# Optimization experiments

Hardware: AMD Instinct MI355X
Metric: run time of the kernel (lower is better)

Reference implementation:

```python
import jax, jax.numpy as jnp
import numpy as np

EPS = 1e-5  # torch LayerNorm default


def _ln(x, g, b):
    m = jnp.mean(x, axis=-1, keepdims=True)
    v = jnp.mean((x - m) ** 2, axis=-1, keepdims=True)
    return (x - m) / jnp.sqrt(v + EPS) * g + b


def setup_inputs() -> dict:
    key = jax.random.key(0)
    ks = jax.random.split(key, 16)
    B, C, H, S, FF, BINS = 2048, 20, 256, 64, 512, 128
    f32 = jnp.float32
    def w(k, shape, s=0.02):
        return jax.random.normal(k, shape, f32) * s
    return {
        "bitplanes": jax.random.normal(ks[0], (B, C, 8, 8), f32),
        "conv1_w": w(ks[1], (H, C, 3, 3), 0.05), "conv1_b": jnp.zeros((H,), f32),
        "conv2_w": w(ks[2], (H, H, 3, 3), 0.05), "conv2_b": jnp.zeros((H,), f32),
        "in_proj_w": w(ks[3], (3 * H, H)), "in_proj_b": jnp.zeros((3 * H,), f32),
        "out_proj_w": w(ks[4], (H, H)), "out_proj_b": jnp.zeros((H,), f32),
        "ln1_g": jnp.ones((H,), f32), "ln1_b": jnp.zeros((H,), f32),
        "ff1_w": w(ks[5], (FF, H)), "ff1_b": jnp.zeros((FF,), f32),
        "ff2_w": w(ks[6], (H, FF)), "ff2_b": jnp.zeros((H,), f32),
        "ln2_g": jnp.ones((H,), f32), "ln2_b": jnp.zeros((H,), f32),
        "be1_w": w(ks[7], (H, H * S)), "be1_b": jnp.zeros((H,), f32),
        "be2_w": w(ks[8], (H, H)), "be2_b": jnp.zeros((H,), f32),
        "L1_w": w(ks[9], (H, 3 * H)), "L1_b": jnp.zeros((H,), f32),
        "L2_w": w(ks[10], (H, H)), "L2_b": jnp.zeros((H,), f32),
        "Lln_g": jnp.ones((H,), f32), "Lln_b": jnp.zeros((H,), f32),
        "H1_w": w(ks[11], (H, 2 * H)), "H1_b": jnp.zeros((H,), f32),
        "H2_w": w(ks[12], (H, H)), "H2_b": jnp.zeros((H,), f32),
        "Hln_g": jnp.ones((H,), f32), "Hln_b": jnp.zeros((H,), f32),
        "v1_w": w(ks[13], (H, H)), "v1_b": jnp.zeros((H,), f32),
        "v2_w": w(ks[14], (BINS, H)), "v2_b": jnp.zeros((BINS,), f32),
    }


def reference(bitplanes, conv1_w, conv1_b, conv2_w, conv2_b,
              in_proj_w, in_proj_b, out_proj_w, out_proj_b,
              ln1_g, ln1_b, ff1_w, ff1_b, ff2_w, ff2_b, ln2_g, ln2_b,
              be1_w, be1_b, be2_w, be2_b,
              L1_w, L1_b, L2_w, L2_b, Lln_g, Lln_b,
              H1_w, H1_b, H2_w, H2_b, Hln_g, Hln_b,
              v1_w, v1_b, v2_w, v2_b):
    N, T, Hd, nh = 8, 8, 256, 4
    B = bitplanes.shape[0]
    dn = ('NCHW', 'OIHW', 'NCHW')
    # conv encoder on 8x8 board
    x = jax.nn.relu(jax.lax.conv_general_dilated(bitplanes, conv1_w, (1, 1), 'SAME', dimension_numbers=dn) + conv1_b[None, :, None, None])
    x = jax.nn.relu(jax.lax.conv_general_dilated(x, conv2_w, (1, 1), 'SAME', dimension_numbers=dn) + conv2_b[None, :, None, None])
    x = x.reshape(B, Hd, 64).transpose(0, 2, 1)  # [B, 64, 256]
    # TransformerEncoderLayer (post-norm, eval mode => dropout off)
    qkv = x @ in_proj_w.T + in_proj_b  # [B, 64, 768]
    q, k, v = jnp.split(qkv, 3, axis=-1)
    dh = Hd // nh
    heads = lambda t: t.reshape(B, 64, nh, dh).transpose(0, 2, 1, 3)
    q, k, v = heads(q), heads(k), heads(v)
    scale = 1.0 / float(dh) ** 0.5
    a = jax.nn.softmax(jnp.einsum('bhqd,bhkd->bhqk', q, k) * scale, axis=-1)
    o = jnp.einsum('bhqk,bhkd->bhqd', a, v).transpose(0, 2, 1, 3).reshape(B, 64, Hd)
    o = o @ out_proj_w.T + out_proj_b
    x = _ln(x + o, ln1_g, ln1_b)
    ff = jax.nn.relu(x @ ff1_w.T + ff1_b) @ ff2_w.T + ff2_b
    x = _ln(x + ff, ln2_g, ln2_b)
    xf = x.reshape(B, 64 * Hd)  # [B, 16384]
    be = jax.nn.relu(jax.nn.relu(xf @ be1_w.T + be1_b) @ be2_w.T + be2_b)

    def Lnet(zL, zH):
        h = jax.nn.relu(jnp.concatenate([zL, zH, be], axis=-1) @ L1_w.T + L1_b)
        return _ln(jax.nn.relu(h @ L2_w.T + L2_b), Lln_g, Lln_b)

    def Hnet(zH, zL):
        h = jax.nn.relu(jnp.concatenate([zH, zL], axis=-1) @ H1_w.T + H1_b)
        return _ln(jax.nn.relu(h @ H2_w.T + H2_b), Hln_g, Hln_b)

    z0 = jnp.zeros((B, Hd), x.dtype)

    def step(carry, i):
        zH, zL = carry
        zL = Lnet(zL, zH)
        zH = jnp.where((i + 1) % T == 0, Hnet(zH, zL), zH)  # H update every T steps
        return (zH, zL), None

    (zH, zL), _ = jax.lax.scan(step, (z0, z0), jnp.arange(N * T - 1))
    zL = Lnet(zL, zH)
    zH = Hnet(zH, zL)
    return jax.nn.relu(zH @ v1_w.T + v1_b) @ v2_w.T + v2_b  # [B, 128]
```

## Files before the change

kernel.cpp:

```cpp
#include <hip/hip_runtime.h>
#include <hip/hip_bf16.h>
#include <math.h>

#define DEV __device__ __forceinline__

typedef __attribute__((ext_vector_type(8))) short s16x8;
typedef __attribute__((ext_vector_type(4))) float f32x4;

DEV f32x4 MF(s16x8 a, s16x8 b, f32x4 c) {
    return __builtin_amdgcn_mfma_f32_16x16x32_bf16(a, b, c, 0, 0, 0);
}

DEV void split3(float x, unsigned short& h, unsigned short& m, unsigned short& l) {
    const unsigned u = __float_as_uint(x);
    h = (unsigned short)(u >> 16);
    const float r1 = x - __uint_as_float(u & 0xffff0000u);
    const unsigned u1 = __float_as_uint(r1);
    m = (unsigned short)(u1 >> 16);
    const float r2 = r1 - __uint_as_float(u1 & 0xffff0000u);
    l = (unsigned short)(__float_as_uint(r2) >> 16);
}

DEV void split8store(const float v[8], unsigned short* d) {
    s16x8 vh, vm, vl;
#pragma unroll
    for (int j = 0; j < 8; ++j) {
        unsigned short h, m, l;
        split3(v[j], h, m, l);
        vh[j] = (short)h; vm[j] = (short)m; vl[j] = (short)l;
    }
    *(s16x8*)(d) = vh;
    *(s16x8*)(d + 512) = vm;
    *(s16x8*)(d + 1024) = vl;
}

DEV void mfma6(f32x4& acc, s16x8 ah, s16x8 am, s16x8 al, const unsigned short* bp) {
    const s16x8 bh = *(const s16x8*)(bp);
    const s16x8 bm = *(const s16x8*)(bp + 512);
    const s16x8 bl = *(const s16x8*)(bp + 1024);
    acc = MF(ah, bh, acc);
    acc = MF(ah, bm, acc);
    acc = MF(am, bh, acc);
    acc = MF(ah, bl, acc);
    acc = MF(al, bh, acc);
    acc = MF(am, bm, acc);
}

__global__ void k_tpose(const float* __restrict__ in, float* __restrict__ out, int N, int K) {
    int total = N * K;
    for (int idx = blockIdx.x * blockDim.x + threadIdx.x; idx < total; idx += gridDim.x * blockDim.x) {
        int n = idx / K, k = idx - n * K;
        out[k * N + n] = in[idx];
    }
}

__global__ void k_wpack3(const float* __restrict__ W, unsigned short* __restrict__ WP,
                         int K, int NT, int ldw, int stride, int off) {
    const int idx = blockIdx.x * 256 + threadIdx.x;
    const int total = (K >> 5) * NT * 64;
    if (idx >= total) return;
    const int lane = idx & 63;
    const int nt = (idx >> 6) % NT;
    const int ks = idx / (64 * NT);
    const int col = nt * 16 + (lane & 15);
    const int k0 = ks * 32 + ((lane >> 4) << 3);
    const float* src = W + (size_t)col * ldw + (size_t)k0 * stride + off;
    float v[8];
#pragma unroll
    for (int j = 0; j < 8; ++j) v[j] = src[j * stride];
    split8store(v, WP + (size_t)((ks * NT + nt) * 3) * 512 + lane * 8);
}

__global__ __launch_bounds__(256) void k_conv1(const float* __restrict__ in, const float* __restrict__ w,
                                               const float* __restrict__ bias, float* __restrict__ out) {
    __shared__ __align__(16) float img[20 * 100];
    __shared__ __align__(16) float stg[16 * 260];
    const int b = blockIdx.x;
    const int t = threadIdx.x;
    for (int idx = t; idx < 2000; idx += 256) {
        int c = idx / 100, pp = idx - c * 100;
        int y = pp / 10, x = pp - y * 10;
        float v = 0.f;
        if (y >= 1 && y <= 8 && x >= 1 && x <= 8)
            v = in[((size_t)b * 20 + c) * 64 + (y - 1) * 8 + (x - 1)];
        img[idx] = v;
    }
    __syncthreads();
    const int oc = t;
    float acc[64];
    const float bz = bias[oc];
#pragma unroll
    for (int p = 0; p < 64; ++p) acc[p] = bz;
    const float* wrow = w + oc * 180;
    for (int c = 0; c < 20; ++c) {
#pragma unroll
        for (int k = 0; k < 9; ++k) {
            const int ky = k / 3, kx = k - ky * 3;
            const float wv = wrow[c * 9 + k];
            const int base = c * 100 + ky * 10 + kx;
#pragma unroll
            for (int p = 0; p < 64; ++p)
                acc[p] = fmaf(wv, img[base + p + ((p >> 3) << 1)], acc[p]);
        }
    }
#pragma unroll
    for (int cc = 0; cc < 4; ++cc) {
        __syncthreads();
#pragma unroll
        for (int p = 0; p < 16; ++p) stg[p * 260 + t] = acc[cc * 16 + p];
        __syncthreads();
        for (int idx = t; idx < 4096; idx += 256) {
            const int r = idx >> 8, c = idx & 255;
            out[((size_t)b * 64 + cc * 16 + r) * 256 + c] = fmaxf(stg[r * 260 + c], 0.f);
        }
    }
}

__global__ __launch_bounds__(256) void k_conv2mf(const float* __restrict__ a1,
                                                 const unsigned short* __restrict__ WPC2,
                                                 const float* __restrict__ bias,
                                                 float* __restrict__ xout,
                                                 unsigned short* __restrict__ xh,
                                                 unsigned short* __restrict__ xm,
                                                 unsigned short* __restrict__ xl) {
    __shared__ __align__(16) unsigned short AhS[100 * 132];
    __shared__ __align__(16) unsigned short AmS[100 * 132];
    __shared__ __align__(16) unsigned short AlS[100 * 132];
    const int b = blockIdx.x, t = threadIdx.x;
    const int wv = t >> 6, lane = t & 63;
    f32x4 acc[16];
#pragma unroll
    for (int nt = 0; nt < 16; ++nt) acc[nt] = (f32x4){0.f, 0.f, 0.f, 0.f};
    const int pl = lane & 15;
    const int py = pl >> 3, px = pl & 7;
    const int akoff = (lane >> 4) << 3;
    for (int h = 0; h < 2; ++h) {
        __syncthreads();
        for (int idx = t; idx < 12800; idx += 256) {
            const int pr = idx >> 7, c = idx & 127;
            const int Y = pr / 10, X = pr - Y * 10;
            float v = 0.f;
            if (Y >= 1 && Y <= 8 && X >= 1 && X <= 8)
                v = a1[((size_t)b * 64 + (Y - 1) * 8 + X - 1) * 256 + h * 128 + c];
            unsigned short hh, mm, ll;
            split3(v, hh, mm, ll);
            AhS[pr * 132 + c] = hh;
            AmS[pr * 132 + c] = mm;
            AlS[pr * 132 + c] = ll;
        }
        __syncthreads();
#pragma unroll
        for (int tap = 0; tap < 9; ++tap) {
            const int dy = tap / 3, dx = tap - dy * 3;
            const int prow = (wv * 2 + py + dy) * 10 + px + dx;
            const unsigned short* arh = AhS + prow * 132 + akoff;
            const unsigned short* arm = AmS + prow * 132 + akoff;
            const unsigned short* arl = AlS + prow * 132 + akoff;
#pragma unroll
            for (int ks = 0; ks < 4; ++ks) {
                const s16x8 ah = *(const s16x8*)(arh + ks * 32);
                const s16x8 am = *(const s16x8*)(arm + ks * 32);
                const s16x8 al = *(const s16x8*)(arl + ks * 32);
                const unsigned short* bp = WPC2 + (size_t)(tap * 128 + (h * 4 + ks) * 16) * 1536 + lane * 8;
#pragma unroll
                for (int nt = 0; nt < 16; ++nt) {
                    mfma6(acc[nt], ah, am, al, bp + nt * 1536);
                }
            }
        }
    }
    const int prow0 = wv * 16 + ((lane >> 4) << 2);
    const int ccol = lane & 15;
#pragma unroll
    for (int nt = 0; nt < 16; ++nt) {
        const float bz = bias[nt * 16 + ccol];
#pragma unroll
        for (int i = 0; i < 4; ++i) {
            const float v = fmaxf(acc[nt][i] + bz, 0.f);
            const size_t o = ((size_t)b * 64 + prow0 + i) * 256 + nt * 16 + ccol;
            xout[o] = v;
            unsigned short hh, mm, ll;
            split3(v, hh, mm, ll);
            xh[o] = hh;
            xm[o] = mm;
            xl[o] = ll;
        }
    }
}

__global__ __launch_bounds__(512) void k_attn2(const float* __restrict__ qkv,
                                               unsigned short* __restrict__ oh, unsigned short* __restrict__ om,
                                               unsigned short* __restrict__ ol) {
    __shared__ __align__(16) float qs[64 * 65];
    __shared__ __align__(16) float ks[64 * 68];
    __shared__ __align__(16) float vs[64 * 68];
    __shared__ float pmax[8 * 64];
    __shared__ float psum[8 * 64];
    const int b = blockIdx.x, h = blockIdx.y;
    const int t = threadIdx.x;
    for (int idx = t; idx < 1024; idx += 512) {
        const int rr = idx >> 4, cc = (idx & 15) * 4;
        const float* src = qkv + ((size_t)b * 64 + rr) * 768 + h * 64 + cc;
        const float4 q4 = *(const float4*)(src);
        const float4 k4 = *(const float4*)(src + 256);
        const float4 v4 = *(const float4*)(src + 512);
        qs[rr * 65 + cc + 0] = q4.x; qs[rr * 65 + cc + 1] = q4.y;
        qs[rr * 65 + cc + 2] = q4.z; qs[rr * 65 + cc + 3] = q4.w;
        *(float4*)(ks + rr * 68 + cc) = k4;
        *(float4*)(vs + rr * 68 + cc) = v4;
    }
    __syncthreads();
    const int r = t & 63;
    const int cg = t >> 6;
    float sc[8];
#pragma unroll
    for (int j = 0; j < 8; ++j) sc[j] = 0.f;
    for (int kk = 0; kk < 64; kk += 4) {
        float qv[4];
#pragma unroll
        for (int i = 0; i < 4; ++i) qv[i] = qs[r * 65 + kk + i];
#pragma unroll
        for (int j = 0; j < 8; ++j) {
            const float4 kv = *(const float4*)(ks + (cg * 8 + j) * 68 + kk);
            sc[j] = fmaf(qv[0], kv.x, sc[j]); sc[j] = fmaf(qv[1], kv.y, sc[j]);
            sc[j] = fmaf(qv[2], kv.z, sc[j]); sc[j] = fmaf(qv[3], kv.w, sc[j]);
        }
    }
    float pm = -1e30f;
#pragma unroll
    for (int j = 0; j < 8; ++j) { sc[j] *= 0.125f; pm = fmaxf(pm, sc[j]); }
    pmax[cg * 64 + r] = pm;
    __syncthreads();
    float m = pmax[r];
#pragma unroll
    for (int i = 1; i < 8; ++i) m = fmaxf(m, pmax[i * 64 + r]);
    float pe[8], ps = 0.f;
#pragma unroll
    for (int j = 0; j < 8; ++j) { pe[j] = __expf(sc[j] - m); ps += pe[j]; }
    psum[cg * 64 + r] = ps;
    __syncthreads();
    float den = psum[r];
#pragma unroll
    for (int i = 1; i < 8; ++i) den += psum[i * 64 + r];
    const float rden = 1.f / den;
#pragma unroll
    for (int j = 0; j < 8; ++j) qs[r * 65 + cg * 8 + j] = pe[j] * rden;
    __syncthreads();
    float oa[8];
#pragma unroll
    for (int j = 0; j < 8; ++j) oa[j] = 0.f;
    for (int c = 0; c < 64; ++c) {
        const float pv = qs[r * 65 + c];
        const float4 v0 = *(const float4*)(vs + c * 68 + cg * 8);
        const float4 v1 = *(const float4*)(vs + c * 68 + cg * 8 + 4);
        oa[0] = fmaf(pv, v0.x, oa[0]); oa[1] = fmaf(pv, v0.y, oa[1]);
        oa[2] = fmaf(pv, v0.z, oa[2]); oa[3] = fmaf(pv, v0.w, oa[3]);
        oa[4] = fmaf(pv, v1.x, oa[4]); oa[5] = fmaf(pv, v1.y, oa[5]);
        oa[6] = fmaf(pv, v1.z, oa[6]); oa[7] = fmaf(pv, v1.w, oa[7]);
    }
#pragma unroll
    for (int j = 0; j < 8; ++j) ks[r * 68 + cg * 8 + j] = oa[j];
    __syncthreads();
    for (int idx = t; idx < 4096; idx += 512) {
        const int rr = idx >> 6, dd = idx & 63;
        const float v = ks[rr * 68 + dd];
        unsigned short hh, mm, ll;
        split3(v, hh, mm, ll);
        const size_t o = ((size_t)b * 64 + rr) * 256 + h * 64 + dd;
        oh[o] = hh;
        om[o] = mm;
        ol[o] = ll;
    }
}

__global__ __launch_bounds__(256) void k_gemm_mf(
    const unsigned short* __restrict__ Ah, const unsigned short* __restrict__ Am,
    const unsigned short* __restrict__ Al,
    const unsigned short* __restrict__ WP, const float* __restrict__ bias,
    float* __restrict__ Cf, unsigned short* __restrict__ Ch, unsigned short* __restrict__ Cm,
    unsigned short* __restrict__ Cl,
    int M, int N, int K, int kChunk, int relu) {
    const int t = threadIdx.x;
    const int wv = t >> 6, lane = t & 63;
    const int row0 = blockIdx.x * 64 + wv * 16;
    const int col0 = blockIdx.y * 64;
    const int NT = N >> 4;
    const int k0 = blockIdx.z * kChunk;
    const int nks = kChunk >> 5;
    f32x4 acc[4];
#pragma unroll
    for (int nt = 0; nt < 4; ++nt) acc[nt] = (f32x4){0.f, 0.f, 0.f, 0.f};
    const int arow = row0 + (lane & 15);
    const size_t aoff = (size_t)arow * K + k0 + ((lane >> 4) << 3);
    const unsigned short* aph = Ah + aoff;
    const unsigned short* apm = Am + aoff;
    const unsigned short* apl = Al + aoff;
    const unsigned short* bp = WP + ((size_t)((k0 >> 5) * NT + (col0 >> 4))) * 1536 + lane * 8;
    const size_t bstride = (size_t)NT * 1536;
    for (int ks = 0; ks < nks; ++ks) {
        const s16x8 ah = *(const s16x8*)aph;
        const s16x8 am = *(const s16x8*)apm;
        const s16x8 al = *(const s16x8*)apl;
        aph += 32; apm += 32; apl += 32;
#pragma unroll
        for (int nt = 0; nt < 4; ++nt) {
            mfma6(acc[nt], ah, am, al, bp + nt * 1536);
        }
        bp += bstride;
    }
    const int crow = row0 + ((lane >> 4) << 2);
    const int ccol = col0 + (lane & 15);
    float bz[4];
#pragma unroll
    for (int nt = 0; nt < 4; ++nt) bz[nt] = bias ? bias[ccol + nt * 16] : 0.f;
    if (Ch) {
#pragma unroll
        for (int nt = 0; nt < 4; ++nt) {
#pragma unroll
            for (int i = 0; i < 4; ++i) {
                float v = acc[nt][i] + bz[nt];
                if (relu) v = fmaxf(v, 0.f);
                unsigned short hh, mm, ll;
                split3(v, hh, mm, ll);
                const size_t o = (size_t)(crow + i) * N + ccol + nt * 16;
                Ch[o] = hh;
                Cm[o] = mm;
                Cl[o] = ll;
            }
        }
    } else {
        float* base = Cf + (size_t)blockIdx.z * M * N;
#pragma unroll
        for (int nt = 0; nt < 4; ++nt) {
#pragma unroll
            for (int i = 0; i < 4; ++i) {
                float v = acc[nt][i] + bz[nt];
                if (relu) v = fmaxf(v, 0.f);
                base[(size_t)(crow + i) * N + ccol + nt * 16] = v;
            }
        }
    }
}

__global__ __launch_bounds__(256) void k_gemm_mf128(
    const unsigned short* __restrict__ Ah, const unsigned short* __restrict__ Am,
    const unsigned short* __restrict__ Al,
    const unsigned short* __restrict__ WP, const float* __restrict__ bias,
    float* __restrict__ Cf, unsigned short* __restrict__ Ch, unsigned short* __restrict__ Cm,
    unsigned short* __restrict__ Cl,
    int M, int N, int K, int relu) {
    const int t = threadIdx.x;
    const int wv = t >> 6, lane = t & 63;
    const int row0 = blockIdx.x * 128 + wv * 32;
    const int col0 = blockIdx.y * 64;
    const int NT = N >> 4;
    const int nks = K >> 5;
    f32x4 acc0[4], acc1[4];
#pragma unroll
    for (int nt = 0; nt < 4; ++nt) {
        acc0[nt] = (f32x4){0.f, 0.f, 0.f, 0.f};
        acc1[nt] = (f32x4){0.f, 0.f, 0.f, 0.f};
    }
    const size_t aoff0 = (size_t)(row0 + (lane & 15)) * K + ((lane >> 4) << 3);
    const size_t aoff1 = aoff0 + (size_t)16 * K;
    const unsigned short* bp = WP + (size_t)(col0 >> 4) * 1536 + lane * 8;
    const size_t bstride = (size_t)NT * 1536;
    for (int ks = 0; ks < nks; ++ks) {
        const size_t ao = ks * 32;
        const s16x8 a0h = *(const s16x8*)(Ah + aoff0 + ao);
        const s16x8 a0m = *(const s16x8*)(Am + aoff0 + ao);
        const s16x8 a0l = *(const s16x8*)(Al + aoff0 + ao);
        const s16x8 a1h = *(const s16x8*)(Ah + aoff1 + ao);
        const s16x8 a1m = *(const s16x8*)(Am + aoff1 + ao);
        const s16x8 a1l = *(const s16x8*)(Al + aoff1 + ao);
#pragma unroll
        for (int nt = 0; nt < 4; ++nt) {
            const unsigned short* bb = bp + nt * 1536;
            const s16x8 bh = *(const s16x8*)(bb);
            const s16x8 bm = *(const s16x8*)(bb + 512);
            const s16x8 bl = *(const s16x8*)(bb + 1024);
            acc0[nt] = MF(a0h, bh, acc0[nt]);
            acc0[nt] = MF(a0h, bm, acc0[nt]);
            acc0[nt] = MF(a0m, bh, acc0[nt]);
            acc0[nt] = MF(a0h, bl, acc0[nt]);
            acc0[nt] = MF(a0l, bh, acc0[nt]);
            acc0[nt] = MF(a0m, bm, acc0[nt]);
            acc1[nt] = MF(a1h, bh, acc1[nt]);
            acc1[nt] = MF(a1h, bm, acc1[nt]);
            acc1[nt] = MF(a1m, bh, acc1[nt]);
            acc1[nt] = MF(a1h, bl, acc1[nt]);
            acc1[nt] = MF(a1l, bh, acc1[nt]);
            acc1[nt] = MF(a1m, bm, acc1[nt]);
        }
        bp += bstride;
    }
    const int crow0 = row0 + ((lane >> 4) << 2);
    const int ccol = col0 + (lane & 15);
    float bz[4];
#pragma unroll
    for (int nt = 0; nt < 4; ++nt) bz[nt] = bias ? bias[ccol + nt * 16] : 0.f;
#pragma unroll
    for (int half = 0; half < 2; ++half) {
        const int crow = crow0 + half * 16;
        f32x4* ac = half ? acc1 : acc0;
        if (Ch) {
#pragma unroll
            for (int nt = 0; nt < 4; ++nt) {
#pragma unroll
                for (int i = 0; i < 4; ++i) {
                    float v = ac[nt][i] + bz[nt];
                    if (relu) v = fmaxf(v, 0.f);
                    unsigned short hh, mm, ll;
                    split3(v, hh, mm, ll);
                    const size_t o = (size_t)(crow + i) * N + ccol + nt * 16;
                    Ch[o] = hh;
                    Cm[o] = mm;
                    Cl[o] = ll;
                }
            }
        } else {
#pragma unroll
            for (int nt = 0; nt < 4; ++nt) {
#pragma unroll
                for (int i = 0; i < 4; ++i) {
                    float v = ac[nt][i] + bz[nt];
                    if (relu) v = fmaxf(v, 0.f);
                    Cf[(size_t)(crow + i) * N + ccol + nt * 16] = v;
                }
            }
        }
    }
}

__global__ __launch_bounds__(256) void k_ln_add(float* __restrict__ x, const float* __restrict__ add,
                                                const float* __restrict__ g, const float* __restrict__ bta,
                                                unsigned short* __restrict__ sh, unsigned short* __restrict__ sm,
                                                unsigned short* __restrict__ sl) {
    const int t = threadIdx.x;
    const size_t r = (size_t)blockIdx.x * 4 + (t >> 6);
    const int lane = t & 63;
    float4 xv = *(const float4*)(x + r * 256 + lane * 4);
    const float4 av = *(const float4*)(add + r * 256 + lane * 4);
    const float4 v = make_float4(xv.x + av.x, xv.y + av.y, xv.z + av.z, xv.w + av.w);
    float s = v.x + v.y + v.z + v.w;
    float ss = fmaf(v.x, v.x, fmaf(v.y, v.y, fmaf(v.z, v.z, v.w * v.w)));
#pragma unroll
    for (int m = 32; m; m >>= 1) { s += __shfl_xor(s, m); ss += __shfl_xor(ss, m); }
    const float mean = s * (1.f / 256.f);
    const float var = ss * (1.f / 256.f) - mean * mean;
    const float rstd = rsqrtf(var + 1e-5f);
    const float4 g4 = *(const float4*)(g + lane * 4);
    const float4 b4 = *(const float4*)(bta + lane * 4);
    float4 ov;
    ov.x = (v.x - mean) * rstd * g4.x + b4.x;
    ov.y = (v.y - mean) * rstd * g4.y + b4.y;
    ov.z = (v.z - mean) * rstd * g4.z + b4.z;
    ov.w = (v.w - mean) * rstd * g4.w + b4.w;
    *(float4*)(x + r * 256 + lane * 4) = ov;
    const float vv[4] = {ov.x, ov.y, ov.z, ov.w};
    unsigned short hh[4], mm[4], ll[4];
#pragma unroll
    for (int j = 0; j < 4; ++j) split3(vv[j], hh[j], mm[j], ll[j]);
    *(ushort4*)(sh + r * 256 + lane * 4) = make_ushort4(hh[0], hh[1], hh[2], hh[3]);
    *(ushort4*)(sm + r * 256 + lane * 4) = make_ushort4(mm[0], mm[1], mm[2], mm[3]);
    *(ushort4*)(sl + r * 256 + lane * 4) = make_ushort4(ll[0], ll[1], ll[2], ll[3]);
}

__global__ void k_be1_reduce(const float* __restrict__ parts, const float* __restrict__ bias,
                             unsigned short* __restrict__ oh, unsigned short* __restrict__ om,
                             unsigned short* __restrict__ ol, int n) {
    const int idx = blockIdx.x * blockDim.x + threadIdx.x;
    if (idx < n) {
        float s = bias[idx & 255];
#pragma unroll
        for (int p = 0; p < 8; ++p) s += parts[(size_t)p * n + idx];
        s = fmaxf(s, 0.f);
        unsigned short hh, mm, ll;
        split3(s, hh, mm, ll);
        oh[idx] = hh;
        om[idx] = mm;
        ol[idx] = ll;
    }
}

DEV void splitpass(const float* scr, unsigned short* frag, int t) {
    const int ks = t >> 6, ln = t & 63;
    const int row = ln & 15;
    const int k0 = ks * 32 + ((ln >> 4) << 3);
    const float* s = scr + row * 260 + k0;
    const float4 p = *(const float4*)s;
    const float4 q = *(const float4*)(s + 4);
    const float v[8] = {p.x, p.y, p.z, p.w, q.x, q.y, q.z, q.w};
    split8store(v, frag + (ks * 3) * 512 + ln * 8);
}

DEV void rungemm(f32x4& a0, f32x4& a1, const unsigned short* __restrict__ WP, int KS,
                 const unsigned short* f0, const unsigned short* f1, const unsigned short* f2,
                 int wv, int lane) {
    for (int ks = 0; ks < KS; ++ks) {
        const unsigned short* fa = (ks < 8) ? f0 : ((ks < 16) ? f1 : f2);
        const int kl = ks & 7;
        const unsigned short* ap = fa + (kl * 3) * 512 + lane * 8;
        const s16x8 ah = *(const s16x8*)(ap);
        const s16x8 am = *(const s16x8*)(ap + 512);
        const s16x8 al = *(const s16x8*)(ap + 1024);
        const unsigned short* bp = WP + (size_t)((ks * 16 + wv * 2) * 3) * 512 + lane * 8;
        mfma6(a0, ah, am, al, bp);
        mfma6(a1, ah, am, al, bp + 1536);
    }
}

DEV void storeC(f32x4 a0, f32x4 a1, const float* __restrict__ bias, float* scr, int wv, int lane) {
    const int rb = (lane >> 4) * 4;
    const int c0 = wv * 32 + (lane & 15);
    const float bz0 = bias[c0];
    const float bz1 = bias[c0 + 16];
    scr[(rb + 0) * 260 + c0] = fmaxf(a0[0] + bz0, 0.f);
    scr[(rb + 1) * 260 + c0] = fmaxf(a0[1] + bz0, 0.f);
    scr[(rb + 2) * 260 + c0] = fmaxf(a0[2] + bz0, 0.f);
    scr[(rb + 3) * 260 + c0] = fmaxf(a0[3] + bz0, 0.f);
    scr[(rb + 0) * 260 + c0 + 16] = fmaxf(a1[0] + bz1, 0.f);
    scr[(rb + 1) * 260 + c0 + 16] = fmaxf(a1[1] + bz1, 0.f);
    scr[(rb + 2) * 260 + c0 + 16] = fmaxf(a1[2] + bz1, 0.f);
    scr[(rb + 3) * 260 + c0 + 16] = fmaxf(a1[3] + bz1, 0.f);
}

DEV void lnpass(float* scr, const float* __restrict__ g, const float* __restrict__ bb, int t) {
    const int row = 2 * (t >> 6) + ((t & 63) >> 5);
    const int c0 = (t & 31) * 8;
    float* s = scr + row * 260 + c0;
    const float4 x0 = *(const float4*)s;
    const float4 x1 = *(const float4*)(s + 4);
    float sum = x0.x + x0.y + x0.z + x0.w + x1.x + x1.y + x1.z + x1.w;
    float sq = fmaf(x0.x, x0.x, fmaf(x0.y, x0.y, fmaf(x0.z, x0.z, x0.w * x0.w)));
    sq = fmaf(x1.x, x1.x, fmaf(x1.y, x1.y, fmaf(x1.z, x1.z, fmaf(x1.w, x1.w, sq))));
#pragma unroll
    for (int m = 16; m; m >>= 1) { sum += __shfl_xor(sum, m); sq += __shfl_xor(sq, m); }
    const float mean = sum * (1.f / 256.f);
    const float var = sq * (1.f / 256.f) - mean * mean;
    const float rstd = rsqrtf(var + 1e-5f);
    const float4 g0 = *(const float4*)(g + c0);
    const float4 g1 = *(const float4*)(g + c0 + 4);
    const float4 b0 = *(const float4*)(bb + c0);
    const float4 b1 = *(const float4*)(bb + c0 + 4);
    float4 o0, o1;
    o0.x = (x0.x - mean) * rstd * g0.x + b0.x;
    o0.y = (x0.y - mean) * rstd * g0.y + b0.y;
    o0.z = (x0.z - mean) * rstd * g0.z + b0.z;
    o0.w = (x0.w - mean) * rstd * g0.w + b0.w;
    o1.x = (x1.x - mean) * rstd * g1.x + b1.x;
    o1.y = (x1.y - mean) * rstd * g1.y + b1.y;
    o1.z = (x1.z - mean) * rstd * g1.z + b1.z;
    o1.w = (x1.w - mean) * rstd * g1.w + b1.w;
    *(float4*)s = o0;
    *(float4*)(s + 4) = o1;
}

__global__ __launch_bounds__(512, 1) void k_hrm(const float* __restrict__ be,
        const unsigned short* __restrict__ L1P, const float* __restrict__ L1b,
        const unsigned short* __restrict__ L2P, const float* __restrict__ L2b,
        const float* __restrict__ Lg, const float* __restrict__ Lbt,
        const unsigned short* __restrict__ H1P, const float* __restrict__ H1b,
        const unsigned short* __restrict__ H2P, const float* __restrict__ H2b,
        const float* __restrict__ Hg, const float* __restrict__ Hbt,
        const unsigned short* __restrict__ v1P, const float* __restrict__ v1b,
        const float* __restrict__ v2T, const float* __restrict__ v2b,
        float* __restrict__ out) {
    __shared__ __align__(16) unsigned short fzL[12288];
    __shared__ __align__(16) unsigned short fzH[12288];
    __shared__ __align__(16) unsigned short fbe[12288];
    __shared__ __align__(16) unsigned short fh1[12288];
    __shared__ __align__(16) float scr[16 * 260];
    const int t = threadIdx.x;
    const int b0 = blockIdx.x * 16;
    const int wv = t >> 6, lane = t & 63;
    for (int i = t; i < 12288; i += 512) { fzL[i] = 0; fzH[i] = 0; }
    {
        const int ks = t >> 6, ln = t & 63;
        const int row = ln & 15;
        const int k0 = ks * 32 + ((ln >> 4) << 3);
        const float* s = be + (size_t)(b0 + row) * 256 + k0;
        const float4 p = *(const float4*)s;
        const float4 q = *(const float4*)(s + 4);
        const float v[8] = {p.x, p.y, p.z, p.w, q.x, q.y, q.z, q.w};
        split8store(v, fbe + (ks * 3) * 512 + ln * 8);
    }
    __syncthreads();
    const f32x4 zero4 = {0.f, 0.f, 0.f, 0.f};
    for (int it = 0; it < 64; ++it) {
        f32x4 a0 = zero4, a1 = zero4;
        rungemm(a0, a1, L1P, 24, fzL, fzH, fbe, wv, lane);
        storeC(a0, a1, L1b, scr, wv, lane);
        __syncthreads();
        splitpass(scr, fh1, t);
        __syncthreads();
        a0 = zero4; a1 = zero4;
        rungemm(a0, a1, L2P, 8, fh1, fh1, fh1, wv, lane);
        storeC(a0, a1, L2b, scr, wv, lane);
        __syncthreads();
        lnpass(scr, Lg, Lbt, t);
        __syncthreads();
        splitpass(scr, fzL, t);
        __syncthreads();
        if (((it + 1) & 7) == 0) {
            a0 = zero4; a1 = zero4;
            rungemm(a0, a1, H1P, 16, fzH, fzL, fzL, wv, lane);
            storeC(a0, a1, H1b, scr, wv, lane);
            __syncthreads();
            splitpass(scr, fh1, t);
            __syncthreads();
            a0 = zero4; a1 = zero4;
            rungemm(a0, a1, H2P, 8, fh1, fh1, fh1, wv, lane);
            storeC(a0, a1, H2b, scr, wv, lane);
            __syncthreads();
            lnpass(scr, Hg, Hbt, t);
            __syncthreads();
            splitpass(scr, fzH, t);
            __syncthreads();
        }
    }
    f32x4 a0 = zero4, a1 = zero4;
    rungemm(a0, a1, v1P, 8, fzH, fzH, fzH, wv, lane);
    storeC(a0, a1, v1b, scr, wv, lane);
    __syncthreads();
    for (int idx = t; idx < 2048; idx += 512) {
        const int r = idx >> 7, oo = idx & 127;
        float s = v2b[oo];
        for (int kk = 0; kk < 256; kk += 4) {
            const float4 c4 = *(const float4*)(&scr[r * 260 + kk]);
            s = fmaf(c4.x, v2T[(kk + 0) * 128 + oo], s);
            s = fmaf(c4.y, v2T[(kk + 1) * 128 + oo], s);
            s = fmaf(c4.z, v2T[(kk + 2) * 128 + oo], s);
            s = fmaf(c4.w, v2T[(kk + 3) * 128 + oo], s);
        }
        out[(size_t)(b0 + r) * 128 + oo] = s;
    }
}

extern "C" void kernel_launch(void* const* d_in, const int* in_sizes, int n_in,
                              void* d_out, int out_size, void* d_ws, size_t ws_size,
                              hipStream_t stream) {
    const float* bitplanes  = (const float*)d_in[0];
    const float* conv1_w    = (const float*)d_in[1];
    const float* conv1_b    = (const float*)d_in[2];
    const float* conv2_w    = (const float*)d_in[3];
    const float* conv2_b    = (const float*)d_in[4];
    const float* in_proj_w  = (const float*)d_in[5];
    const float* in_proj_b  = (const float*)d_in[6];
    const float* out_proj_w = (const float*)d_in[7];
    const float* out_proj_b = (const float*)d_in[8];
    const float* ln1_g      = (const float*)d_in[9];
    const float* ln1_b      = (const float*)d_in[10];
    const float* ff1_w      = (const float*)d_in[11];
    const float* ff1_b      = (const float*)d_in[12];
    const float* ff2_w      = (const float*)d_in[13];
    const float* ff2_b      = (const float*)d_in[14];
    const float* ln2_g      = (const float*)d_in[15];
    const float* ln2_b      = (const float*)d_in[16];
    const float* be1_w      = (const float*)d_in[17];
    const float* be1_b      = (const float*)d_in[18];
    const float* be2_w      = (const float*)d_in[19];
    const float* be2_b      = (const float*)d_in[20];
    const float* L1_w       = (const float*)d_in[21];
    const float* L1_b       = (const float*)d_in[22];
    const float* L2_w       = (const float*)d_in[23];
    const float* L2_b       = (const float*)d_in[24];
    const float* Lln_g      = (const float*)d_in[25];
    const float* Lln_b      = (const float*)d_in[26];
    const float* H1_w       = (const float*)d_in[27];
    const float* H1_b       = (const float*)d_in[28];
    const float* H2_w       = (const float*)d_in[29];
    const float* H2_b       = (const float*)d_in[30];
    const float* Hln_g      = (const float*)d_in[31];
    const float* Hln_b      = (const float*)d_in[32];
    const float* v1_w       = (const float*)d_in[33];
    const float* v1_b       = (const float*)d_in[34];
    const float* v2_w       = (const float*)d_in[35];
    const float* v2_b       = (const float*)d_in[36];

    const size_t persist = 9404416ull;
    int CB = 64;
    for (int c = 2048; c >= 64; c >>= 1) {
        size_t needBytes = ((size_t)c * 106880ull + persist) * 4ull;
        if (needBytes <= ws_size) { CB = c; break; }
    }
    const int NCH = 2048 / CB;

    float* ws = (float*)d_ws;
    float* a1buf = ws;
    float* xbuf  = a1buf + (size_t)CB * 16384;
    float* sbuf  = xbuf + (size_t)CB * 16384;
    float* tbuf  = sbuf + (size_t)CB * 24576;
    float* bemf  = tbuf + (size_t)CB * 49152;
    float* wpQf  = bemf + (size_t)CB * 384;
    float* v2T   = wpQf + 294912;
    float* L1Pf  = v2T + 32768;
    float* L2Pf  = L1Pf + 294912;
    float* H1Pf  = L2Pf + 98304;
    float* H2Pf  = H1Pf + 196608;
    float* v1Pf  = H2Pf + 98304;
    float* beB   = v1Pf + 98304;
    float* wpOf  = beB + 524288;
    float* wpF1f = wpOf + 98304;
    float* wpF2f = wpF1f + 196608;
    float* wpB1f = wpF2f + 196608;
    float* wpB2f = wpB1f + 6291456;
    float* wpC2f = wpB2f + 98304;

    unsigned short* soh = (unsigned short*)sbuf;
    unsigned short* som = soh + (size_t)CB * 16384;
    unsigned short* sol = som + (size_t)CB * 16384;
    unsigned short* tbh = (unsigned short*)tbuf;
    unsigned short* tbm = tbh + (size_t)CB * 32768;
    unsigned short* tbl = tbm + (size_t)CB * 32768;
    unsigned short* bemh = (unsigned short*)bemf;
    unsigned short* bemm = bemh + (size_t)CB * 256;
    unsigned short* beml = bemm + (size_t)CB * 256;
    unsigned short* wpQ = (unsigned short*)wpQf;
    unsigned short* L1P = (unsigned short*)L1Pf;
    unsigned short* L2P = (unsigned short*)L2Pf;
    unsigned short* H1P = (unsigned short*)H1Pf;
    unsigned short* H2P = (unsigned short*)H2Pf;
    unsigned short* v1P = (unsigned short*)v1Pf;
    unsigned short* wpO = (unsigned short*)wpOf;
    unsigned short* wpF1 = (unsigned short*)wpF1f;
    unsigned short* wpF2 = (unsigned short*)wpF2f;
    unsigned short* wpB1 = (unsigned short*)wpB1f;
    unsigned short* wpB2 = (unsigned short*)wpB2f;
    unsigned short* wpC2 = (unsigned short*)wpC2f;

    k_tpose<<<64, 256, 0, stream>>>(v2_w, v2T, 128, 256);
    k_wpack3<<<96, 256, 0, stream>>>(in_proj_w, wpQ, 256, 48, 256, 1, 0);
    k_wpack3<<<96, 256, 0, stream>>>(L1_w, L1P, 768, 16, 768, 1, 0);
    k_wpack3<<<32, 256, 0, stream>>>(L2_w, L2P, 256, 16, 256, 1, 0);
    k_wpack3<<<64, 256, 0, stream>>>(H1_w, H1P, 512, 16, 512, 1, 0);
    k_wpack3<<<32, 256, 0, stream>>>(H2_w, H2P, 256, 16, 256, 1, 0);
    k_wpack3<<<32, 256, 0, stream>>>(v1_w, v1P, 256, 16, 256, 1, 0);
    k_wpack3<<<32, 256, 0, stream>>>(out_proj_w, wpO, 256, 16, 256, 1, 0);
    k_wpack3<<<64, 256, 0, stream>>>(ff1_w, wpF1, 256, 32, 256, 1, 0);
    k_wpack3<<<64, 256, 0, stream>>>(ff2_w, wpF2, 512, 16, 512, 1, 0);
    k_wpack3<<<2048, 256, 0, stream>>>(be1_w, wpB1, 16384, 16, 16384, 1, 0);
    k_wpack3<<<32, 256, 0, stream>>>(be2_w, wpB2, 256, 16, 256, 1, 0);
    for (int tap = 0; tap < 9; ++tap)
        k_wpack3<<<32, 256, 0, stream>>>(conv2_w, wpC2 + (size_t)tap * 196608, 256, 16, 2304, 9, tap);

    for (int ch = 0; ch < NCH; ++ch) {
        const float* bp_c = bitplanes + (size_t)ch * CB * 20 * 64;
        k_conv1<<<CB, 256, 0, stream>>>(bp_c, conv1_w, conv1_b, a1buf);
        k_conv2mf<<<CB, 256, 0, stream>>>(a1buf, wpC2, conv2_b, xbuf, soh, som, sol);
        k_gemm_mf128<<<dim3(CB / 2, 12), 256, 0, stream>>>(soh, som, sol, wpQ, in_proj_b,
                                                           tbuf, nullptr, nullptr, nullptr,
                                                           CB * 64, 768, 256, 0);
        k_attn2<<<dim3(CB, 4), 512, 0, stream>>>(tbuf, soh, som, sol);
        k_gemm_mf128<<<dim3(CB / 2, 4), 256, 0, stream>>>(soh, som, sol, wpO, out_proj_b,
                                                          a1buf, nullptr, nullptr, nullptr,
                                                          CB * 64, 256, 256, 0);
        k_ln_add<<<CB * 16, 256, 0, stream>>>(xbuf, a1buf, ln1_g, ln1_b, soh, som, sol);
        k_gemm_mf128<<<dim3(CB / 2, 8), 256, 0, stream>>>(soh, som, sol, wpF1, ff1_b,
                                                          nullptr, tbh, tbm, tbl,
                                                          CB * 64, 512, 256, 1);
        k_gemm_mf128<<<dim3(CB / 2, 4), 256, 0, stream>>>(tbh, tbm, tbl, wpF2, ff2_b,
                                                          a1buf, nullptr, nullptr, nullptr,
                                                          CB * 64, 256, 512, 0);
        k_ln_add<<<CB * 16, 256, 0, stream>>>(xbuf, a1buf, ln2_g, ln2_b, soh, som, sol);
        k_gemm_mf<<<dim3(CB / 64, 4, 8), 256, 0, stream>>>(soh, som, sol, wpB1, nullptr,
                                                           tbuf, nullptr, nullptr, nullptr,
                                                           CB, 256, 16384, 2048, 0);
        k_be1_reduce<<<CB, 256, 0, stream>>>(tbuf, be1_b, bemh, bemm, beml, CB * 256);
        k_gemm_mf<<<dim3(CB / 64, 4, 1), 256, 0, stream>>>(bemh, bemm, beml, wpB2, be2_b,
                                                           beB + (size_t)ch * CB * 256, nullptr, nullptr, nullptr,
                                                           CB, 256, 256, 256, 1);
    }

    k_hrm<<<128, 512, 0, stream>>>(beB, L1P, L1_b, L2P, L2_b, Lln_g, Lln_b,
                                   H1P, H1_b, H2P, H2_b, Hln_g, Hln_b,
                                   v1P, v1_b, v2T, v2_b, (float*)d_out);
}
```

Baseline: 5.038 ms.

## Keep HRM activations as fp32 in LDS and split to bf16x3 inside GEMM

Activations (zL, zH, be, h1) now stay in shared memory as fp32, and each wave splits its A fragment into three bf16 parts right before the MFMAs. This removes the separate split passes over pre-split bf16x3 fragment buffers, and their barriers, from each recurrent step. It also shrinks LDS use, and launch bounds now ask for two blocks per CU. The cost is that every wave repeats the split arithmetic in the inner GEMM loop. The tighter register budget from the new launch bounds could also cause spills, and with only 128 blocks the extra occupancy may not be usable.

```diff
diff --git a/kernel.cpp b/kernel.cpp
--- a/kernel.cpp
+++ b/kernel.cpp
@@ -483,52 +483,52 @@
     }
 }
 
-DEV void splitpass(const float* scr, unsigned short* frag, int t) {
-    const int ks = t >> 6, ln = t & 63;
-    const int row = ln & 15;
-    const int k0 = ks * 32 + ((ln >> 4) << 3);
-    const float* s = scr + row * 260 + k0;
-    const float4 p = *(const float4*)s;
-    const float4 q = *(const float4*)(s + 4);
+DEV void loadsplitA(const float* z, int kl, int lane, s16x8& ah, s16x8& am, s16x8& al) {
+    const int row = lane & 15;
+    const int k0 = kl * 32 + ((lane >> 4) << 3);
+    const float4 p = *(const float4*)(z + row * 260 + k0);
+    const float4 q = *(const float4*)(z + row * 260 + k0 + 4);
     const float v[8] = {p.x, p.y, p.z, p.w, q.x, q.y, q.z, q.w};
-    split8store(v, frag + (ks * 3) * 512 + ln * 8);
+#pragma unroll
+    for (int j = 0; j < 8; ++j) {
+        unsigned short h, m, l;
+        split3(v[j], h, m, l);
+        ah[j] = (short)h; am[j] = (short)m; al[j] = (short)l;
+    }
 }
 
 DEV void rungemm(f32x4& a0, f32x4& a1, const unsigned short* __restrict__ WP, int KS,
-                 const unsigned short* f0, const unsigned short* f1, const unsigned short* f2,
+                 const float* z0, const float* z1, const float* z2,
                  int wv, int lane) {
     for (int ks = 0; ks < KS; ++ks) {
-        const unsigned short* fa = (ks < 8) ? f0 : ((ks < 16) ? f1 : f2);
-        const int kl = ks & 7;
-        const unsigned short* ap = fa + (kl * 3) * 512 + lane * 8;
-        const s16x8 ah = *(const s16x8*)(ap);
-        const s16x8 am = *(const s16x8*)(ap + 512);
-        const s16x8 al = *(const s16x8*)(ap + 1024);
+        const float* za = (ks < 8) ? z0 : ((ks < 16) ? z1 : z2);
+        s16x8 ah, am, al;
+        loadsplitA(za, ks & 7, lane, ah, am, al);
         const unsigned short* bp = WP + (size_t)((ks * 16 + wv * 2) * 3) * 512 + lane * 8;
         mfma6(a0, ah, am, al, bp);
         mfma6(a1, ah, am, al, bp + 1536);
     }
 }
 
-DEV void storeC(f32x4 a0, f32x4 a1, const float* __restrict__ bias, float* scr, int wv, int lane) {
+DEV void storeC(f32x4 a0, f32x4 a1, const float* __restrict__ bias, float* dst, int wv, int lane) {
     const int rb = (lane >> 4) * 4;
     const int c0 = wv * 32 + (lane & 15);
     const float bz0 = bias[c0];
     const float bz1 = bias[c0 + 16];
-    scr[(rb + 0) * 260 + c0] = fmaxf(a0[0] + bz0, 0.f);
-    scr[(rb + 1) * 260 + c0] = fmaxf(a0[1] + bz0, 0.f);
-    scr[(rb + 2) * 260 + c0] = fmaxf(a0[2] + bz0, 0.f);
-    scr[(rb + 3) * 260 + c0] = fmaxf(a0[3] + bz0, 0.f);
-    scr[(rb + 0) * 260 + c0 + 16] = fmaxf(a1[0] + bz1, 0.f);
-    scr[(rb + 1) * 260 + c0 + 16] = fmaxf(a1[1] + bz1, 0.f);
-    scr[(rb + 2) * 260 + c0 + 16] = fmaxf(a1[2] + bz1, 0.f);
-    scr[(rb + 3) * 260 + c0 + 16] = fmaxf(a1[3] + bz1, 0.f);
-}
-
-DEV void lnpass(float* scr, const float* __restrict__ g, const float* __restrict__ bb, int t) {
+    dst[(rb + 0) * 260 + c0] = fmaxf(a0[0] + bz0, 0.f);
+    dst[(rb + 1) * 260 + c0] = fmaxf(a0[1] + bz0, 0.f);
+    dst[(rb + 2) * 260 + c0] = fmaxf(a0[2] + bz0, 0.f);
+    dst[(rb + 3) * 260 + c0] = fmaxf(a0[3] + bz0, 0.f);
+    dst[(rb + 0) * 260 + c0 + 16] = fmaxf(a1[0] + bz1, 0.f);
+    dst[(rb + 1) * 260 + c0 + 16] = fmaxf(a1[1] + bz1, 0.f);
+    dst[(rb + 2) * 260 + c0 + 16] = fmaxf(a1[2] + bz1, 0.f);
+    dst[(rb + 3) * 260 + c0 + 16] = fmaxf(a1[3] + bz1, 0.f);
+}
+
+DEV void lnpass(float* zbuf, const float* __restrict__ g, const float* __restrict__ bb, int t) {
     const int row = 2 * (t >> 6) + ((t & 63) >> 5);
     const int c0 = (t & 31) * 8;
-    float* s = scr + row * 260 + c0;
+    float* s = zbuf + row * 260 + c0;
     const float4 x0 = *(const float4*)s;
     const float4 x1 = *(const float4*)(s + 4);
     float sum = x0.x + x0.y + x0.z + x0.w + x1.x + x1.y + x1.z + x1.w;
@@ -556,7 +556,7 @@
     *(float4*)(s + 4) = o1;
 }
 
-__global__ __launch_bounds__(512, 1) void k_hrm(const float* __restrict__ be,
+__global__ __launch_bounds__(512, 2) void k_hrm(const float* __restrict__ be,
         const unsigned short* __restrict__ L1P, const float* __restrict__ L1b,
         const unsigned short* __restrict__ L2P, const float* __restrict__ L2b,
         const float* __restrict__ Lg, const float* __restrict__ Lbt,
@@ -566,68 +566,55 @@
         const unsigned short* __restrict__ v1P, const float* __restrict__ v1b,
         const float* __restrict__ v2T, const float* __restrict__ v2b,
         float* __restrict__ out) {
-    __shared__ __align__(16) unsigned short fzL[12288];
-    __shared__ __align__(16) unsigned short fzH[12288];
-    __shared__ __align__(16) unsigned short fbe[12288];
-    __shared__ __align__(16) unsigned short fh1[12288];
-    __shared__ __align__(16) float scr[16 * 260];
+    __shared__ __align__(16) float zL[16 * 260];
+    __shared__ __align__(16) float zH[16 * 260];
+    __shared__ __align__(16) float beS[16 * 260];
+    __shared__ __align__(16) float h1[16 * 260];
     const int t = threadIdx.x;
     const int b0 = blockIdx.x * 16;
     const int wv = t >> 6, lane = t & 63;
-    for (int i = t; i < 12288; i += 512) { fzL[i] = 0; fzH[i] = 0; }
-    {
-        const int ks = t >> 6, ln = t & 63;
-        const int row = ln & 15;
-        const int k0 = ks * 32 + ((ln >> 4) << 3);
-        const float* s = be + (size_t)(b0 + row) * 256 + k0;
-        const float4 p = *(const float4*)s;
-        const float4 q = *(const float4*)(s + 4);
-        const float v[8] = {p.x, p.y, p.z, p.w, q.x, q.y, q.z, q.w};
-        split8store(v, fbe + (ks * 3) * 512 + ln * 8);
+    for (int i = t; i < 4160; i += 512) { zL[i] = 0.f; zH[i] = 0.f; }
+    for (int idx = t; idx < 2048; idx += 512) {
+        const int r = idx >> 7, c = idx & 127;
+        const float2 v = *(const float2*)(be + (size_t)(b0 + r) * 256 + c * 2);
+        beS[r * 260 + c * 2] = v.x;
+        beS[r * 260 + c * 2 + 1] = v.y;
     }
     __syncthreads();
     const f32x4 zero4 = {0.f, 0.f, 0.f, 0.f};
     for (int it = 0; it < 64; ++it) {
         f32x4 a0 = zero4, a1 = zero4;
-        rungemm(a0, a1, L1P, 24, fzL, fzH, fbe, wv, lane);
-        storeC(a0, a1, L1b, scr, wv, lane);
-        __syncthreads();
-        splitpass(scr, fh1, t);
+        rungemm(a0, a1, L1P, 24, zL, zH, beS, wv, lane);
+        storeC(a0, a1, L1b, h1, wv, lane);
         __syncthreads();
         a0 = zero4; a1 = zero4;
-        rungemm(a0, a1, L2P, 8, fh1, fh1, fh1, wv, lane);
-        storeC(a0, a1, L2b, scr, wv, lane);
+        rungemm(a0, a1, L2P, 8, h1, h1, h1, wv, lane);
+        storeC(a0, a1, L2b, zL, wv, lane);
         __syncthreads();
-        lnpass(scr, Lg, Lbt, t);
-        __syncthreads();
-        splitpass(scr, fzL, t);
+        lnpass(zL, Lg, Lbt, t);
         __syncthreads();
         if (((it + 1) & 7) == 0) {
             a0 = zero4; a1 = zero4;
-            rungemm(a0, a1, H1P, 16, fzH, fzL, fzL, wv, lane);
-            storeC(a0, a1, H1b, scr, wv, lane);
-            __syncthreads();
-            splitpass(scr, fh1, t);
+            rungemm(a0, a1, H1P, 16, zH, zL, zL, wv, lane);
+            storeC(a0, a1, H1b, h1, wv, lane);
             __syncthreads();
             a0 = zero4; a1 = zero4;
-            rungemm(a0, a1, H2P, 8, fh1, fh1, fh1, wv, lane);
-            storeC(a0, a1, H2b, scr, wv, lane);
+            rungemm(a0, a1, H2P, 8, h1, h1, h1, wv, lane);
+            storeC(a0, a1, H2b, zH, wv, lane);
             __syncthreads();
-            lnpass(scr, Hg, Hbt, t);
+            lnpass(zH, Hg, Hbt, t);
             __syncthreads();
-            splitpass(scr, fzH, t);
-            __syncthreads();
         }
     }
     f32x4 a0 = zero4, a1 = zero4;
-    rungemm(a0, a1, v1P, 8, fzH, fzH, fzH, wv, lane);
-    storeC(a0, a1, v1b, scr, wv, lane);
+    rungemm(a0, a1, v1P, 8, zH, zH, zH, wv, lane);
+    storeC(a0, a1, v1b, h1, wv, lane);
     __syncthreads();
     for (int idx = t; idx < 2048; idx += 512) {
         const int r = idx >> 7, oo = idx & 127;
         float s = v2b[oo];
         for (int kk = 0; kk < 256; kk += 4) {
-            const float4 c4 = *(const float4*)(&scr[r * 260 + kk]);
+            const float4 c4 = *(const float4*)(&h1[r * 260 + kk]);
             s = fmaf(c4.x, v2T[(kk + 0) * 128 + oo], s);
             s = fmaf(c4.y, v2T[(kk + 1) * 128 + oo], s);
             s = fmaf(c4.z, v2T[(kk + 2) * 128 + oo], s);
```

Measured after the change: 5.291 ms. 5.0% more time.
